# Kernel tuning notes

Hardware: AMD Instinct MI355X
Metric: run time of the kernel (lower is better)

Reference implementation:

```python
import jax, jax.numpy as jnp
import numpy as np

N_HEAD = 16
NEG = -10000.0


def setup_inputs() -> dict:
    key = jax.random.key(0)
    k1, k2, k3 = jax.random.split(key, 3)
    B, S, NX = 2, 2048, 1024
    x = jax.random.normal(k1, (B, S, NX), dtype=jnp.float32)
    # Conv1D weights: y = x @ W + b (HF Conv1D stores weight as [in, out])
    w_attn = jax.random.normal(k2, (NX, 3 * NX), dtype=jnp.float32) * 0.02
    b_attn = jnp.zeros((3 * NX,), dtype=jnp.float32)
    w_proj = jax.random.normal(k3, (NX, NX), dtype=jnp.float32) * 0.02
    b_proj = jnp.zeros((NX,), dtype=jnp.float32)
    return {"x": x, "w_attn": w_attn, "b_attn": b_attn,
            "w_proj": w_proj, "b_proj": b_proj}


def reference(x, w_attn, b_attn, w_proj, b_proj):
    B, S, NX = x.shape
    H = N_HEAD
    D = NX // H  # head dim
    qkv = x @ w_attn + b_attn                      # [B, S, 3*NX]
    q, k, v = jnp.split(qkv, 3, axis=-1)
    # split heads -> [B, H, S, D]
    q = q.reshape(B, S, H, D).transpose(0, 2, 1, 3)
    k = k.reshape(B, S, H, D).transpose(0, 2, 1, 3)
    v = v.reshape(B, S, H, D).transpose(0, 2, 1, 3)
    # scores [B, H, S, S], scaled (scale=True)
    w = jnp.einsum('bhqd,bhkd->bhqk', q, k) / jnp.sqrt(jnp.asarray(D, x.dtype))
    # causal additive mask exactly as the torch code: w*b + NEG*(1-b)
    bias = jnp.tril(jnp.ones((S, S), dtype=x.dtype))[None, None]  # [1,1,S,S]
    w = w * bias + NEG * (1.0 - bias)
    w = jax.nn.softmax(w, axis=-1)
    a = jnp.einsum('bhqk,bhkd->bhqd', w, v)        # [B, H, S, D]
    a = a.transpose(0, 2, 1, 3).reshape(B, S, NX)  # merge heads
    return a @ w_proj + b_proj
```

## Files before the change

kernel.cpp:

```cpp
#include <hip/hip_runtime.h>
#include <cstdint>
#include <cstddef>


typedef __bf16 bf16;
typedef __bf16 bf16x8 __attribute__((ext_vector_type(8)));
typedef __bf16 bf16x4 __attribute__((ext_vector_type(4)));
typedef float f32x4 __attribute__((ext_vector_type(4)));

#define MFMA16(a, b, c) __builtin_amdgcn_mfma_f32_16x16x32_bf16(a, b, c, 0, 0, 0)

typedef const __attribute__((address_space(1))) void* gas_ptr;
typedef __attribute__((address_space(3))) void* las_ptr;
__device__ __forceinline__ void async16(const void* g, void* l) {
    __builtin_amdgcn_global_load_lds((gas_ptr)g, (las_ptr)l, 16, 0, 0);
}
__device__ __forceinline__ float exp2f_fast(float x) { return __builtin_amdgcn_exp2f(x); }

__global__ __launch_bounds__(256) void prep_kernel(const float* __restrict__ x, bf16* __restrict__ xb,
                                                   const float* __restrict__ wa, bf16* __restrict__ wTa,
                                                   const float* __restrict__ wp, bf16* __restrict__ wTp) {
    __shared__ float tile[32][33];
    const int bid = blockIdx.x, tid = threadIdx.x;
    if (bid < 4096) {
        int i = (bid * 256 + tid) * 4;
        float4 v = *reinterpret_cast<const float4*>(x + i);
        bf16x4 o;
        o[0] = (bf16)v.x; o[1] = (bf16)v.y; o[2] = (bf16)v.z; o[3] = (bf16)v.w;
        *reinterpret_cast<bf16x4*>(xb + i) = o;
        return;
    }
    const float* in; bf16* out; int N, t;
    if (bid < 7168) { t = bid - 4096; in = wa; out = wTa; N = 3072; }
    else            { t = bid - 7168; in = wp; out = wTp; N = 1024; }
    const int K = 1024;
    int bx = t % (N >> 5), by = t / (N >> 5);
    int n0 = bx * 32, k0 = by * 32, tx = tid & 31, ty = tid >> 5;
#pragma unroll
    for (int i = 0; i < 32; i += 8)
        tile[ty + i][tx] = in[(size_t)(k0 + ty + i) * N + n0 + tx];
    __syncthreads();
#pragma unroll
    for (int i = 0; i < 32; i += 8)
        out[(size_t)(n0 + ty + i) * K + k0 + tx] = (bf16)tile[tx][ty + i];
}

template <int OUT_BF16>
__global__ __launch_bounds__(256) void gemm_kernel(const bf16* __restrict__ A,
                                                   const bf16* __restrict__ Bt,
                                                   const float* __restrict__ bias,
                                                   void* __restrict__ Cout,
                                                   int M, int N, int K) {
    __shared__ bf16 Alds[2][128 * 32];
    __shared__ bf16 Blds[2][128 * 32];
    const int tid = threadIdx.x;
    const int w = tid >> 6, l = tid & 63;
    const int lane16 = l & 15, quad = l >> 4;
    const int wr = w >> 1, wc = w & 1;
    const int row0 = blockIdx.y * 128, col0 = blockIdx.x * 128;

    const int e = tid * 8;
    const int sr = e >> 5, sc = e & 31;

    f32x4 zero4 = {0.f, 0.f, 0.f, 0.f};
    f32x4 acc[4][4];
#pragma unroll
    for (int i = 0; i < 4; ++i)
#pragma unroll
        for (int j = 0; j < 4; ++j) acc[i][j] = zero4;

#pragma unroll
    for (int ch = 0; ch < 2; ++ch) {
        async16(A + (size_t)(row0 + ch * 64 + sr) * K + sc, &Alds[0][ch * 2048 + e]);
        async16(Bt + (size_t)(col0 + ch * 64 + sr) * K + sc, &Blds[0][ch * 2048 + e]);
    }

    const int niter = K >> 5;
    for (int it = 0; it < niter; ++it) {
        const int cur = it & 1;
        __syncthreads();
        if (it + 1 < niter) {
            const int k1 = (it + 1) << 5;
#pragma unroll
            for (int ch = 0; ch < 2; ++ch) {
                async16(A + (size_t)(row0 + ch * 64 + sr) * K + k1 + sc, &Alds[cur ^ 1][ch * 2048 + e]);
                async16(Bt + (size_t)(col0 + ch * 64 + sr) * K + k1 + sc, &Blds[cur ^ 1][ch * 2048 + e]);
            }
        }
        bf16x8 af[4], bfr[4];
#pragma unroll
        for (int i = 0; i < 4; ++i) {
            af[i] = *reinterpret_cast<const bf16x8*>(&Alds[cur][(64 * wr + 16 * i + lane16) * 32 + quad * 8]);
            bfr[i] = *reinterpret_cast<const bf16x8*>(&Blds[cur][(64 * wc + 16 * i + lane16) * 32 + quad * 8]);
        }
#pragma unroll
        for (int i = 0; i < 4; ++i)
#pragma unroll
            for (int j = 0; j < 4; ++j) acc[i][j] = MFMA16(af[i], bfr[j], acc[i][j]);
    }

#pragma unroll
    for (int i = 0; i < 4; ++i)
#pragma unroll
        for (int j = 0; j < 4; ++j)
#pragma unroll
            for (int r = 0; r < 4; ++r) {
                int row = row0 + 64 * wr + 16 * i + quad * 4 + r;
                int col = col0 + 64 * wc + 16 * j + lane16;
                float v = acc[i][j][r] + bias[col];
                if (OUT_BF16)
                    reinterpret_cast<bf16*>(Cout)[(size_t)row * N + col] = (bf16)v;
                else
                    reinterpret_cast<float*>(Cout)[(size_t)row * N + col] = v;
            }
}

template <int OUT_BF16>
__global__ __launch_bounds__(256) void gemm64k_kernel(const bf16* __restrict__ A,
                                                      const bf16* __restrict__ Bt,
                                                      const float* __restrict__ bias,
                                                      void* __restrict__ Cout,
                                                      int M, int N, int K) {
    __shared__ bf16 Alds[2][64 * 64];
    __shared__ bf16 Blds[2][128 * 64];
    const int tid = threadIdx.x;
    const int w = tid >> 6, l = tid & 63;
    const int lane16 = l & 15, quad = l >> 4;
    const int wr = w >> 1, wc = w & 1;
    const int row0 = blockIdx.y * 64, col0 = blockIdx.x * 128;

    f32x4 zero4 = {0.f, 0.f, 0.f, 0.f};
    f32x4 acc[2][4];
#pragma unroll
    for (int i = 0; i < 2; ++i)
#pragma unroll
        for (int j = 0; j < 4; ++j) acc[i][j] = zero4;

    auto stage = [&](int buf, int k0) {
#pragma unroll
        for (int c = 0; c < 2; ++c) {
            int idx = c * 256 + tid;
            int r = idx >> 3, cc = idx & 7, gc = cc ^ (r & 7);
            async16(A + (size_t)(row0 + r) * K + k0 + gc * 8, &Alds[buf][idx * 8]);
        }
#pragma unroll
        for (int c = 0; c < 4; ++c) {
            int idx = c * 256 + tid;
            int r = idx >> 3, cc = idx & 7, gc = cc ^ (r & 7);
            async16(Bt + (size_t)(col0 + r) * K + k0 + gc * 8, &Blds[buf][idx * 8]);
        }
    };

    stage(0, 0);
    const int niter = K >> 6;
    for (int it = 0; it < niter; ++it) {
        const int cur = it & 1;
        __syncthreads();
        if (it + 1 < niter) stage(cur ^ 1, (it + 1) << 6);
        bf16x8 af[2][2], bfr[4][2];
#pragma unroll
        for (int i = 0; i < 2; ++i) {
            int r = 32 * wr + 16 * i + lane16;
#pragma unroll
            for (int ks = 0; ks < 2; ++ks) {
                int cc = (quad + 4 * ks) ^ (r & 7);
                af[i][ks] = *reinterpret_cast<const bf16x8*>(&Alds[cur][r * 64 + cc * 8]);
            }
        }
#pragma unroll
        for (int j = 0; j < 4; ++j) {
            int r = 64 * wc + 16 * j + lane16;
#pragma unroll
            for (int ks = 0; ks < 2; ++ks) {
                int cc = (quad + 4 * ks) ^ (r & 7);
                bfr[j][ks] = *reinterpret_cast<const bf16x8*>(&Blds[cur][r * 64 + cc * 8]);
            }
        }
#pragma unroll
        for (int ks = 0; ks < 2; ++ks)
#pragma unroll
            for (int i = 0; i < 2; ++i)
#pragma unroll
                for (int j = 0; j < 4; ++j) acc[i][j] = MFMA16(af[i][ks], bfr[j][ks], acc[i][j]);
    }

#pragma unroll
    for (int i = 0; i < 2; ++i)
#pragma unroll
        for (int j = 0; j < 4; ++j)
#pragma unroll
            for (int r = 0; r < 4; ++r) {
                int row = row0 + 32 * wr + 16 * i + quad * 4 + r;
                int col = col0 + 64 * wc + 16 * j + lane16;
                float v = acc[i][j][r] + bias[col];
                if (OUT_BF16)
                    reinterpret_cast<bf16*>(Cout)[(size_t)row * N + col] = (bf16)v;
                else
                    reinterpret_cast<float*>(Cout)[(size_t)row * N + col] = v;
            }
}

__global__ __launch_bounds__(256) void attn_kernel(const bf16* __restrict__ qkv,
                                                   bf16* __restrict__ aout) {
    const int S = 2048;
    const int bh = blockIdx.x;
    const int b = bh >> 4, h = bh & 15;
    const int rr = blockIdx.y >> 3, j = blockIdx.y & 7;
    const int qt = (rr == 0) ? (31 - j) : (rr == 1) ? (16 + j) : (rr == 2) ? (15 - j) : j;
    const int nkt = qt + 1;
    const int tid = threadIdx.x, w = tid >> 6, l = tid & 63;
    const int lane16 = l & 15, quad = l >> 4;

    __shared__ bf16 Klds[64 * 72];
    __shared__ bf16 Vt[64 * 72];
    __shared__ bf16 Plds[4][16 * 72];

    const bf16* base = qkv + (size_t)b * S * 3072;
    const float qscale = 0.125f * 1.4426950408889634f;
    const float NEGs = -10000.0f * 1.4426950408889634f;

    bf16x8 qf[2];
#pragma unroll
    for (int hv = 0; hv < 2; ++hv) {
        const bf16* qp = base + (size_t)(qt * 64 + 16 * w + lane16) * 3072 + h * 64;
        bf16x8 t = *reinterpret_cast<const bf16x8*>(qp + hv * 32 + quad * 8);
#pragma unroll
        for (int jj = 0; jj < 8; ++jj) t[jj] = (bf16)((float)t[jj] * qscale);
        qf[hv] = t;
    }

    f32x4 zero4 = {0.f, 0.f, 0.f, 0.f};
    f32x4 o[4];
#pragma unroll
    for (int df = 0; df < 4; ++df) o[df] = zero4;
    float lsum = 0.f;

    const int kr = tid >> 3, kc = (tid & 7) * 8;
    const int vp = tid & 31, vd = (tid >> 5) * 8;
    bf16x8 kreg0, kreg1, vreg0, vreg1;
    auto load_tile = [&](int kt) {
        const bf16* tb = base + (size_t)(kt * 64) * 3072;
        kreg0 = *reinterpret_cast<const bf16x8*>(tb + (size_t)kr * 3072 + 1024 + h * 64 + kc);
        kreg1 = *reinterpret_cast<const bf16x8*>(tb + (size_t)(32 + kr) * 3072 + 1024 + h * 64 + kc);
        vreg0 = *reinterpret_cast<const bf16x8*>(tb + (size_t)(2 * vp) * 3072 + 2048 + h * 64 + vd);
        vreg1 = *reinterpret_cast<const bf16x8*>(tb + (size_t)(2 * vp + 1) * 3072 + 2048 + h * 64 + vd);
    };

    load_tile(0);
    for (int kt = 0; kt < nkt; ++kt) {
        __syncthreads();
        *reinterpret_cast<bf16x8*>(&Klds[kr * 72 + kc]) = kreg0;
        *reinterpret_cast<bf16x8*>(&Klds[(32 + kr) * 72 + kc]) = kreg1;
#pragma unroll
        for (int jj = 0; jj < 8; ++jj) {
            union { bf16 h2[2]; uint32_t u; } pk;
            pk.h2[0] = vreg0[jj]; pk.h2[1] = vreg1[jj];
            *reinterpret_cast<uint32_t*>(&Vt[(vd + jj) * 72 + 2 * vp]) = pk.u;
        }
        __syncthreads();
        if (kt + 1 < nkt) load_tile(kt + 1);

        f32x4 st[4];
#pragma unroll
        for (int kf = 0; kf < 4; ++kf) {
            bf16x8 k0 = *reinterpret_cast<const bf16x8*>(&Klds[(kf * 16 + lane16) * 72 + quad * 8]);
            bf16x8 k1 = *reinterpret_cast<const bf16x8*>(&Klds[(kf * 16 + lane16) * 72 + 32 + quad * 8]);
            f32x4 z = zero4;
            z = MFMA16(k0, qf[0], z);
            z = MFMA16(k1, qf[1], z);
            st[kf] = z;
        }

        if (kt == qt) {
            const int q = qt * 64 + 16 * w + lane16;
#pragma unroll
            for (int kf = 0; kf < 4; ++kf)
#pragma unroll
                for (int r = 0; r < 4; ++r)
                    if (kt * 64 + kf * 16 + quad * 4 + r > q) st[kf][r] = NEGs;
        }

        float rs = 0.f;
        bf16* Prow = &Plds[w][lane16 * 72];
#pragma unroll
        for (int kf = 0; kf < 4; ++kf) {
            bf16x4 pk;
#pragma unroll
            for (int r = 0; r < 4; ++r) {
                float pv = exp2f_fast(st[kf][r]);
                rs += pv;
                pk[r] = (bf16)pv;
            }
            *reinterpret_cast<bf16x4*>(Prow + kf * 16 + quad * 4) = pk;
        }
        lsum += rs;

#pragma unroll
        for (int kf2 = 0; kf2 < 2; ++kf2) {
            bf16x8 pf = *reinterpret_cast<const bf16x8*>(
                &Plds[w][lane16 * 72 + kf2 * 32 + quad * 8]);
#pragma unroll
            for (int df = 0; df < 4; ++df) {
                bf16x8 vf = *reinterpret_cast<const bf16x8*>(
                    &Vt[(df * 16 + lane16) * 72 + kf2 * 32 + quad * 8]);
                o[df] = MFMA16(pf, vf, o[df]);
            }
        }
    }

    lsum += __shfl_xor(lsum, 16, 64);
    lsum += __shfl_xor(lsum, 32, 64);
    float inv = 1.0f / lsum;

#pragma unroll
    for (int r = 0; r < 4; ++r) {
        float li = __shfl(inv, quad * 4 + r, 64);
        int row = qt * 64 + 16 * w + quad * 4 + r;
#pragma unroll
        for (int df = 0; df < 4; ++df)
            aout[(size_t)(b * S + row) * 1024 + h * 64 + df * 16 + lane16] =
                (bf16)(o[df][r] * li);
    }
}

extern "C" void kernel_launch(void* const* d_in, const int* in_sizes, int n_in,
                              void* d_out, int out_size, void* d_ws, size_t ws_size,
                              hipStream_t stream) {
    const float* x      = (const float*)d_in[0];
    const float* w_attn = (const float*)d_in[1];
    const float* b_attn = (const float*)d_in[2];
    const float* w_proj = (const float*)d_in[3];
    const float* b_proj = (const float*)d_in[4];
    float* out = (float*)d_out;
    char* ws = (char*)d_ws;

    const int Mtok = 4096, NX = 1024, N3 = 3072;
    bf16* xb   = (bf16*)(ws);
    bf16* wTa  = (bf16*)(ws + ((size_t)8 << 20));
    bf16* wTp  = (bf16*)(ws + ((size_t)14 << 20));
    bf16* qkv  = (bf16*)(ws + ((size_t)16 << 20));
    bf16* abuf = (bf16*)(ws + ((size_t)40 << 20));

    prep_kernel<<<dim3(8192), 256, 0, stream>>>(x, xb, w_attn, wTa, w_proj, wTp);
    gemm_kernel<1><<<dim3(N3 / 128, Mtok / 128), 256, 0, stream>>>(xb, wTa, b_attn, qkv, Mtok, N3, NX);
    attn_kernel<<<dim3(32, 32), 256, 0, stream>>>(qkv, abuf);
    gemm64k_kernel<0><<<dim3(NX / 128, Mtok / 64), 256, 0, stream>>>(abuf, wTp, b_proj, out, Mtok, NX, NX);
}
```

Baseline: 171.0 us.

## Process two query tiles per attention block to reuse K/V tiles

Each attention block now handles 128 query rows, as two 64-row halves with separate accumulators, instead of 64. Every K/V tile loaded into LDS and every K/V fragment read into registers is reused for both halves, halving K/V global traffic per query and the grid size. The cost is higher register pressure (double accumulators plus preloaded K/V fragments), a larger P buffer in LDS, fewer blocks (512), and coarser causal load balance.

```diff
diff --git a/kernel.cpp b/kernel.cpp
--- a/kernel.cpp
+++ b/kernel.cpp
@@ -204,46 +204,51 @@
                                                    bf16* __restrict__ aout) {
     const int S = 2048;
     const int bh = blockIdx.x;
-    const int b = bh >> 4, h = bh & 15;
+    const int b = bh >> 4, hd = bh & 15;
     const int rr = blockIdx.y >> 3, j = blockIdx.y & 7;
-    const int qt = (rr == 0) ? (31 - j) : (rr == 1) ? (16 + j) : (rr == 2) ? (15 - j) : j;
-    const int nkt = qt + 1;
+    const int qt = (rr == 0) ? (15 - j) : j;
+    const int nkt = 2 * qt + 2;
     const int tid = threadIdx.x, w = tid >> 6, l = tid & 63;
     const int lane16 = l & 15, quad = l >> 4;
 
     __shared__ bf16 Klds[64 * 72];
     __shared__ bf16 Vt[64 * 72];
-    __shared__ bf16 Plds[4][16 * 72];
+    __shared__ bf16 Plds[4][2][16 * 72];
 
     const bf16* base = qkv + (size_t)b * S * 3072;
     const float qscale = 0.125f * 1.4426950408889634f;
     const float NEGs = -10000.0f * 1.4426950408889634f;
 
-    bf16x8 qf[2];
-#pragma unroll
-    for (int hv = 0; hv < 2; ++hv) {
-        const bf16* qp = base + (size_t)(qt * 64 + 16 * w + lane16) * 3072 + h * 64;
-        bf16x8 t = *reinterpret_cast<const bf16x8*>(qp + hv * 32 + quad * 8);
-#pragma unroll
-        for (int jj = 0; jj < 8; ++jj) t[jj] = (bf16)((float)t[jj] * qscale);
-        qf[hv] = t;
+    bf16x8 qf[2][2];
+#pragma unroll
+    for (int qh = 0; qh < 2; ++qh) {
+        const bf16* qp = base + (size_t)(qt * 128 + 64 * qh + 16 * w + lane16) * 3072 + hd * 64;
+#pragma unroll
+        for (int hv = 0; hv < 2; ++hv) {
+            bf16x8 t = *reinterpret_cast<const bf16x8*>(qp + hv * 32 + quad * 8);
+#pragma unroll
+            for (int jj = 0; jj < 8; ++jj) t[jj] = (bf16)((float)t[jj] * qscale);
+            qf[qh][hv] = t;
+        }
     }
 
     f32x4 zero4 = {0.f, 0.f, 0.f, 0.f};
-    f32x4 o[4];
-#pragma unroll
-    for (int df = 0; df < 4; ++df) o[df] = zero4;
-    float lsum = 0.f;
+    f32x4 o[2][4];
+    float lsum[2] = {0.f, 0.f};
+#pragma unroll
+    for (int qh = 0; qh < 2; ++qh)
+#pragma unroll
+        for (int df = 0; df < 4; ++df) o[qh][df] = zero4;
 
     const int kr = tid >> 3, kc = (tid & 7) * 8;
     const int vp = tid & 31, vd = (tid >> 5) * 8;
     bf16x8 kreg0, kreg1, vreg0, vreg1;
     auto load_tile = [&](int kt) {
         const bf16* tb = base + (size_t)(kt * 64) * 3072;
-        kreg0 = *reinterpret_cast<const bf16x8*>(tb + (size_t)kr * 3072 + 1024 + h * 64 + kc);
-        kreg1 = *reinterpret_cast<const bf16x8*>(tb + (size_t)(32 + kr) * 3072 + 1024 + h * 64 + kc);
-        vreg0 = *reinterpret_cast<const bf16x8*>(tb + (size_t)(2 * vp) * 3072 + 2048 + h * 64 + vd);
-        vreg1 = *reinterpret_cast<const bf16x8*>(tb + (size_t)(2 * vp + 1) * 3072 + 2048 + h * 64 + vd);
+        kreg0 = *reinterpret_cast<const bf16x8*>(tb + (size_t)kr * 3072 + 1024 + hd * 64 + kc);
+        kreg1 = *reinterpret_cast<const bf16x8*>(tb + (size_t)(32 + kr) * 3072 + 1024 + hd * 64 + kc);
+        vreg0 = *reinterpret_cast<const bf16x8*>(tb + (size_t)(2 * vp) * 3072 + 2048 + hd * 64 + vd);
+        vreg1 = *reinterpret_cast<const bf16x8*>(tb + (size_t)(2 * vp + 1) * 3072 + 2048 + hd * 64 + vd);
     };
 
     load_tile(0);
@@ -260,66 +265,84 @@
         __syncthreads();
         if (kt + 1 < nkt) load_tile(kt + 1);
 
-        f32x4 st[4];
+        bf16x8 kfrag[4][2];
 #pragma unroll
         for (int kf = 0; kf < 4; ++kf) {
-            bf16x8 k0 = *reinterpret_cast<const bf16x8*>(&Klds[(kf * 16 + lane16) * 72 + quad * 8]);
-            bf16x8 k1 = *reinterpret_cast<const bf16x8*>(&Klds[(kf * 16 + lane16) * 72 + 32 + quad * 8]);
-            f32x4 z = zero4;
-            z = MFMA16(k0, qf[0], z);
-            z = MFMA16(k1, qf[1], z);
-            st[kf] = z;
-        }
-
-        if (kt == qt) {
-            const int q = qt * 64 + 16 * w + lane16;
-#pragma unroll
-            for (int kf = 0; kf < 4; ++kf)
-#pragma unroll
-                for (int r = 0; r < 4; ++r)
-                    if (kt * 64 + kf * 16 + quad * 4 + r > q) st[kf][r] = NEGs;
-        }
-
-        float rs = 0.f;
-        bf16* Prow = &Plds[w][lane16 * 72];
-#pragma unroll
-        for (int kf = 0; kf < 4; ++kf) {
-            bf16x4 pk;
-#pragma unroll
-            for (int r = 0; r < 4; ++r) {
-                float pv = exp2f_fast(st[kf][r]);
-                rs += pv;
-                pk[r] = (bf16)pv;
-            }
-            *reinterpret_cast<bf16x4*>(Prow + kf * 16 + quad * 4) = pk;
-        }
-        lsum += rs;
-
-#pragma unroll
-        for (int kf2 = 0; kf2 < 2; ++kf2) {
-            bf16x8 pf = *reinterpret_cast<const bf16x8*>(
-                &Plds[w][lane16 * 72 + kf2 * 32 + quad * 8]);
-#pragma unroll
-            for (int df = 0; df < 4; ++df) {
-                bf16x8 vf = *reinterpret_cast<const bf16x8*>(
+            kfrag[kf][0] = *reinterpret_cast<const bf16x8*>(&Klds[(kf * 16 + lane16) * 72 + quad * 8]);
+            kfrag[kf][1] = *reinterpret_cast<const bf16x8*>(&Klds[(kf * 16 + lane16) * 72 + 32 + quad * 8]);
+        }
+        bf16x8 vfrag[2][4];
+#pragma unroll
+        for (int kf2 = 0; kf2 < 2; ++kf2)
+#pragma unroll
+            for (int df = 0; df < 4; ++df)
+                vfrag[kf2][df] = *reinterpret_cast<const bf16x8*>(
                     &Vt[(df * 16 + lane16) * 72 + kf2 * 32 + quad * 8]);
-                o[df] = MFMA16(pf, vf, o[df]);
-            }
-        }
-    }
-
-    lsum += __shfl_xor(lsum, 16, 64);
-    lsum += __shfl_xor(lsum, 32, 64);
-    float inv = 1.0f / lsum;
-
-#pragma unroll
-    for (int r = 0; r < 4; ++r) {
-        float li = __shfl(inv, quad * 4 + r, 64);
-        int row = qt * 64 + 16 * w + quad * 4 + r;
-#pragma unroll
-        for (int df = 0; df < 4; ++df)
-            aout[(size_t)(b * S + row) * 1024 + h * 64 + df * 16 + lane16] =
-                (bf16)(o[df][r] * li);
+
+#pragma unroll
+        for (int qh = 0; qh < 2; ++qh) {
+            const int dtile = 2 * qt + qh;
+            if (kt > dtile) continue;
+
+            f32x4 st[4];
+#pragma unroll
+            for (int kf = 0; kf < 4; ++kf) {
+                f32x4 z = zero4;
+                z = MFMA16(kfrag[kf][0], qf[qh][0], z);
+                z = MFMA16(kfrag[kf][1], qf[qh][1], z);
+                st[kf] = z;
+            }
+
+            if (kt == dtile) {
+                const int q = qt * 128 + 64 * qh + 16 * w + lane16;
+#pragma unroll
+                for (int kf = 0; kf < 4; ++kf)
+#pragma unroll
+                    for (int r = 0; r < 4; ++r)
+                        if (kt * 64 + kf * 16 + quad * 4 + r > q) st[kf][r] = NEGs;
+            }
+
+            float rs = 0.f;
+            bf16* Prow = &Plds[w][qh][lane16 * 72];
+#pragma unroll
+            for (int kf = 0; kf < 4; ++kf) {
+                bf16x4 pk;
+#pragma unroll
+                for (int r = 0; r < 4; ++r) {
+                    float pv = exp2f_fast(st[kf][r]);
+                    rs += pv;
+                    pk[r] = (bf16)pv;
+                }
+                *reinterpret_cast<bf16x4*>(Prow + kf * 16 + quad * 4) = pk;
+            }
+            lsum[qh] += rs;
+
+#pragma unroll
+            for (int kf2 = 0; kf2 < 2; ++kf2) {
+                bf16x8 pf = *reinterpret_cast<const bf16x8*>(
+                    &Plds[w][qh][lane16 * 72 + kf2 * 32 + quad * 8]);
+#pragma unroll
+                for (int df = 0; df < 4; ++df)
+                    o[qh][df] = MFMA16(pf, vfrag[kf2][df], o[qh][df]);
+            }
+        }
+    }
+
+#pragma unroll
+    for (int qh = 0; qh < 2; ++qh) {
+        float ls = lsum[qh];
+        ls += __shfl_xor(ls, 16, 64);
+        ls += __shfl_xor(ls, 32, 64);
+        float inv = 1.0f / ls;
+#pragma unroll
+        for (int r = 0; r < 4; ++r) {
+            float li = __shfl(inv, quad * 4 + r, 64);
+            int row = qt * 128 + 64 * qh + 16 * w + quad * 4 + r;
+#pragma unroll
+            for (int df = 0; df < 4; ++df)
+                aout[(size_t)(b * S + row) * 1024 + hd * 64 + df * 16 + lane16] =
+                    (bf16)(o[qh][df][r] * li);
+        }
     }
 }
 
@@ -343,6 +366,6 @@
 
     prep_kernel<<<dim3(8192), 256, 0, stream>>>(x, xb, w_attn, wTa, w_proj, wTp);
     gemm_kernel<1><<<dim3(N3 / 128, Mtok / 128), 256, 0, stream>>>(xb, wTa, b_attn, qkv, Mtok, N3, NX);
-    attn_kernel<<<dim3(32, 32), 256, 0, stream>>>(qkv, abuf);
+    attn_kernel<<<dim3(32, 16), 256, 0, stream>>>(qkv, abuf);
     gemm64k_kernel<0><<<dim3(NX / 128, Mtok / 64), 256, 0, stream>>>(abuf, wTp, b_proj, out, Mtok, NX, NX);
 }
```

New measurement: 181.3 us. +6.1%, slower.
